# Kernel optimization log

Hardware: AMD Instinct MI355X
Metric: run time of the kernel (lower is better)

Reference implementation:

```python
import jax, jax.numpy as jnp
import numpy as np

B, N, H, D = 16, 512, 8, 128  # batch, nodes, heads, hid_dim (per-head dim == hid_dim)


def setup_inputs() -> dict:
    key = jax.random.key(0)
    ks = jax.random.split(key, 12)
    x = jax.random.normal(ks[0], (B, N, D), dtype=jnp.float32)
    dist = jax.random.normal(ks[1], (B, N, N), dtype=jnp.float32)
    mask = (jax.random.uniform(ks[2], (B, N)) < 0.9).astype(jnp.float32)
    w_std = 0.02
    Wq = jax.random.normal(ks[3], (D, H * D), dtype=jnp.float32) * w_std
    Wk = jax.random.normal(ks[4], (D, H * D), dtype=jnp.float32) * w_std
    Wv = jax.random.normal(ks[5], (D, H * D), dtype=jnp.float32) * w_std
    Wo = jax.random.normal(ks[6], (H * D, D), dtype=jnp.float32) * w_std
    bq = jax.random.normal(ks[7], (H * D,), dtype=jnp.float32) * w_std
    bk = jax.random.normal(ks[8], (H * D,), dtype=jnp.float32) * w_std
    bv = jax.random.normal(ks[9], (H * D,), dtype=jnp.float32) * w_std
    bo = jax.random.normal(ks[10], (D,), dtype=jnp.float32) * w_std
    return {"x": x, "dist": dist, "mask": mask,
            "Wq": Wq, "bq": bq, "Wk": Wk, "bk": bk,
            "Wv": Wv, "bv": bv, "Wo": Wo, "bo": bo}


def reference(x, dist, mask, Wq, bq, Wk, bk, Wv, bv, Wo, bo):
    scale = jnp.asarray(D, x.dtype) ** -0.5
    # projections: [B,N,H*D] -> [B,H,N,D]
    q = (x @ Wq + bq).reshape(B, N, H, D).transpose(0, 2, 1, 3)
    k = (x @ Wk + bk).reshape(B, N, H, D).transpose(0, 2, 1, 3)
    v = (x @ Wv + bv).reshape(B, N, H, D).transpose(0, 2, 1, 3)
    m = mask[:, None, :, None]  # [B,1,N,1]
    q = q * m * scale
    k = k * m
    v = v * m
    a = jnp.einsum('bhnd,bhmd->bhnm', q, k)  # [B,H,N,N]
    a = a + dist[:, None, :, :]  # dist bias broadcast over heads
    amask = (mask[:, :, None] * mask[:, None, :])[:, None, :, :]  # [B,1,N,N]
    a = jnp.where(amask == 0, jnp.asarray(-1e9, a.dtype), a)
    a = jax.nn.softmax(a, axis=-1)
    a = jnp.where(amask == 0, jnp.asarray(0.0, a.dtype), a)
    y = jnp.einsum('bhnm,bhmd->bhnd', a, v)
    y = y.transpose(0, 2, 1, 3).reshape(B, N, H * D)
    y = y @ Wo + bo
    return y * mask[:, :, None]
```

## Files before the change

### kernel.cpp

```cpp
#include <hip/hip_runtime.h>
#include <hip/hip_bf16.h>

#define B_ 16
#define N_ 512
#define H_ 8
#define D_ 128
#define HD_ 1024
#define SCALE_ 0.08838834764831845f

typedef __attribute__((ext_vector_type(8))) short bf16x8;
typedef __attribute__((ext_vector_type(4))) float f32x4;
typedef __attribute__((ext_vector_type(4))) _Float16 f16x4;

__device__ __forceinline__ unsigned short f2bf(float f) {
    union { __hip_bfloat16 h; unsigned short u; } cv;
    cv.h = __float2bfloat16(f);
    return cv.u;
}
__device__ __forceinline__ unsigned short f2h(float f) {
    union { _Float16 h; unsigned short u; } cv;
    cv.h = (_Float16)f;
    return cv.u;
}

#define BAR_LIGHT() do {                                     \
    asm volatile("s_waitcnt lgkmcnt(0)" ::: "memory");       \
    __builtin_amdgcn_s_barrier();                            \
    asm volatile("" ::: "memory");                           \
} while (0)

__global__ __launch_bounds__(256) void prep_kernel(
    const float* __restrict__ Wq, const float* __restrict__ Wk,
    const float* __restrict__ Wv, const float* __restrict__ Wo,
    const float* __restrict__ x,
    unsigned short* __restrict__ wTh, unsigned short* __restrict__ woT,
    unsigned short* __restrict__ xh)
{
    __shared__ float T[32][33];
    const int tile = blockIdx.x;
    const int t = threadIdx.x;
    if (tile < 384) {
        const int w = tile / 128;
        const int rem = tile % 128;
        const int kt = rem & 3;
        const int ct = rem >> 2;
        const float* W = (w == 0) ? Wq : (w == 1) ? Wk : Wv;
        const int k0 = kt * 32, c0 = ct * 32;
        #pragma unroll
        for (int u = 0; u < 4; u++) {
            int lin = t + 256 * u; int r = lin >> 5, c = lin & 31;
            T[r][c] = W[(size_t)(k0 + r) * 1024 + c0 + c];
        }
        __syncthreads();
        unsigned short* oh = wTh + (size_t)w * 131072;
        #pragma unroll
        for (int u = 0; u < 4; u++) {
            int lin = t + 256 * u; int c = lin >> 5, r = lin & 31;
            oh[(size_t)(c0 + c) * 128 + k0 + r] = f2bf(T[r][c]);
        }
    } else if (tile < 512) {
        const int rem = tile - 384;
        const int nt = rem & 3;
        const int kt = rem >> 2;
        const int k0 = kt * 32, n0 = nt * 32;
        #pragma unroll
        for (int u = 0; u < 4; u++) {
            int lin = t + 256 * u; int r = lin >> 5, c = lin & 31;
            T[r][c] = Wo[(size_t)(k0 + r) * 128 + n0 + c];
        }
        __syncthreads();
        #pragma unroll
        for (int u = 0; u < 4; u++) {
            int lin = t + 256 * u; int c = lin >> 5, r = lin & 31;
            woT[(size_t)(n0 + c) * 1024 + k0 + r] = f2bf(T[r][c]);
        }
    } else {
        const size_t base = (size_t)(tile - 512) * 2048 + (size_t)t * 8;
        float4 v0 = *(const float4*)&x[base];
        float4 v1 = *(const float4*)&x[base + 4];
        union { bf16x8 v; unsigned short s[8]; } H;
        H.s[0] = f2bf(v0.x); H.s[1] = f2bf(v0.y);
        H.s[2] = f2bf(v0.z); H.s[3] = f2bf(v0.w);
        H.s[4] = f2bf(v1.x); H.s[5] = f2bf(v1.y);
        H.s[6] = f2bf(v1.z); H.s[7] = f2bf(v1.w);
        *(bf16x8*)&xh[base] = H.v;
    }
}

__global__ __launch_bounds__(256, 3) void qkv_kernel(
    const unsigned short* __restrict__ xh, const float* __restrict__ mask,
    const unsigned short* __restrict__ wTh,
    const float* __restrict__ bq, const float* __restrict__ bk,
    const float* __restrict__ bv,
    unsigned short* __restrict__ q, unsigned short* __restrict__ k,
    unsigned short* __restrict__ vT)
{
    const int cb = blockIdx.x % 24;
    const int by = blockIdx.x / 24;
    const int row0 = by * 128, c0 = cb * 128;
    const int which = c0 >> 10, w0 = c0 & 1023;
    const float* bi = (which == 0) ? bq : (which == 1) ? bk : bv;

    __shared__ alignas(16) unsigned short Wh[128][136];
    __shared__ float biS[128];
    __shared__ float mskS[128];

    const int t = threadIdx.x;
    if (t < 128) { biS[t] = bi[w0 + t]; mskS[t] = mask[row0 + t]; }

    const unsigned short* whp = wTh + (size_t)which * 131072 + (size_t)w0 * 128;
    #pragma unroll
    for (int u = 0; u < 8; u++) {
        int lin = t + 256 * u; int c = lin >> 4, k8 = (lin & 15) * 8;
        *(bf16x8*)&Wh[c][k8] = *(const bf16x8*)&whp[(size_t)c * 128 + k8];
    }

    const int wave = t >> 6, lane = t & 63, m16 = lane & 15, g4 = lane >> 4;
    const int rw = row0 + wave * 32;

    bf16x8 ah[2][4];
    #pragma unroll
    for (int mt = 0; mt < 2; mt++)
        #pragma unroll
        for (int kc = 0; kc < 4; kc++)
            ah[mt][kc] = *(const bf16x8*)&xh[(size_t)(rw + mt * 16 + m16) * 128 + kc * 32 + g4 * 8];
    __syncthreads();

    const f32x4 zero = {0.f, 0.f, 0.f, 0.f};
    f32x4 acc[2][8];
    #pragma unroll
    for (int mt = 0; mt < 2; mt++)
        #pragma unroll
        for (int nt = 0; nt < 8; nt++) acc[mt][nt] = zero;

    #pragma unroll
    for (int nt = 0; nt < 8; nt++) {
        #pragma unroll
        for (int kc = 0; kc < 4; kc++) {
            bf16x8 bh = *(const bf16x8*)&Wh[nt * 16 + m16][kc * 32 + g4 * 8];
            #pragma unroll
            for (int mt = 0; mt < 2; mt++)
                acc[mt][nt] = __builtin_amdgcn_mfma_f32_16x16x32_bf16(ah[mt][kc], bh, acc[mt][nt], 0, 0, 0);
        }
    }
    __syncthreads();

    const int b = row0 >> 9, h = w0 >> 7;
    const int iseq0 = row0 & 511;
    unsigned short* Tr = &Wh[0][0];

    if (which == 2) {
        #pragma unroll
        for (int mt = 0; mt < 2; mt++)
            #pragma unroll
            for (int nt = 0; nt < 8; nt++)
                #pragma unroll
                for (int r = 0; r < 4; r++) {
                    int rowl = wave * 32 + mt * 16 + g4 * 4 + r;
                    int col = nt * 16 + m16;
                    Tr[col * 136 + rowl] = f2h((acc[mt][nt][r] + biS[col]) * mskS[rowl]);
                }
        __syncthreads();
        unsigned short* vbase = vT + (size_t)(b * 8 + h) * 128 * 512 + iseq0;
        #pragma unroll
        for (int u = 0; u < 8; u++) {
            int lin = t + 256 * u; int dl = lin >> 4, i8 = (lin & 15) * 8;
            *(bf16x8*)&vbase[(size_t)dl * 512 + i8] = *(const bf16x8*)&Tr[dl * 136 + i8];
        }
    } else {
        const float sc = (which == 0) ? SCALE_ : 1.0f;
        #pragma unroll
        for (int mt = 0; mt < 2; mt++)
            #pragma unroll
            for (int nt = 0; nt < 8; nt++)
                #pragma unroll
                for (int r = 0; r < 4; r++) {
                    int rowl = wave * 32 + mt * 16 + g4 * 4 + r;
                    int col = nt * 16 + m16;
                    Tr[rowl * 136 + col] = f2bf((acc[mt][nt][r] + biS[col]) * (mskS[rowl] * sc));
                }
        __syncthreads();
        unsigned short* dst = ((which == 0) ? q : k) +
                              ((size_t)(b * 8 + h) * 512 + iseq0) * 128;
        #pragma unroll
        for (int u = 0; u < 8; u++) {
            int lin = t + 256 * u; int rl = lin >> 4, c8 = (lin & 15) * 8;
            *(bf16x8*)&dst[(size_t)rl * 128 + c8] = *(const bf16x8*)&Tr[rl * 136 + c8];
        }
    }
}

__global__ __launch_bounds__(256, 2) void attn_kernel(
    const unsigned short* __restrict__ q, const unsigned short* __restrict__ k,
    const unsigned short* __restrict__ vT, const float* __restrict__ dist,
    const float* __restrict__ mask, unsigned short* __restrict__ y)
{
    const int xid = blockIdx.x;
    const int b = (xid & 7) | ((xid >> 8) << 3);
    const int itile = (xid >> 3) & 3;
    const int h = (xid >> 5) & 7;
    const int bh = b * 8 + h;
    const int i0 = itile * 128;

    const unsigned short* qb = q + (size_t)bh * 512 * 128;
    const unsigned short* kb = k + (size_t)bh * 512 * 128;
    const unsigned short* vb = vT + (size_t)bh * 128 * 512;

    __shared__ alignas(16) unsigned short Ks[2][64][136];
    __shared__ alignas(16) unsigned short Vs[2][128][76];
    __shared__ alignas(16) float cmS[512];

    const int t = threadIdx.x;
    const int wave = t >> 6, lane = t & 63;
    const int m16 = lane & 15, g4 = lane >> 4;
    const int iw = i0 + wave * 32;

    cmS[t] = (mask[b * 512 + t] == 0.0f) ? -1e9f : 0.0f;
    cmS[256 + t] = (mask[b * 512 + 256 + t] == 0.0f) ? -1e9f : 0.0f;

    bf16x8 aq0[4], aq1[4];
    #pragma unroll
    for (int c = 0; c < 4; c++) {
        aq0[c] = *(const bf16x8*)(qb + (size_t)(iw + m16) * 128 + c * 32 + g4 * 8);
        aq1[c] = *(const bf16x8*)(qb + (size_t)(iw + 16 + m16) * 128 + c * 32 + g4 * 8);
    }

    const int krow = t >> 2, kcol = (t & 3) * 32;
    const int vrow = t >> 1, vcol = (t & 1) * 32;

    const float* dbase = dist + ((size_t)b * 512 + iw) * 512;

    bf16x8 kp[4], vp[4];
    #pragma unroll
    for (int u = 0; u < 4; u++) {
        kp[u] = *(const bf16x8*)(kb + (size_t)krow * 128 + kcol + u * 8);
        vp[u] = *(const bf16x8*)(vb + (size_t)vrow * 512 + vcol + u * 8);
    }
    #pragma unroll
    for (int u = 0; u < 4; u++) {
        *(bf16x8*)&Ks[0][krow][kcol + u * 8] = kp[u];
        union { bf16x8 v8; ushort4 h4[2]; } cv; cv.v8 = vp[u];
        *(ushort4*)&Vs[0][vrow][vcol + u * 8] = cv.h4[0];
        *(ushort4*)&Vs[0][vrow][vcol + u * 8 + 4] = cv.h4[1];
    }
    BAR_LIGHT();

    const f32x4 zero = {0.f, 0.f, 0.f, 0.f};
    float rl0 = 0.f, rl1 = 0.f;
    f32x4 Ot0[8] = {zero, zero, zero, zero, zero, zero, zero, zero};
    f32x4 Ot1[8] = {zero, zero, zero, zero, zero, zero, zero, zero};

    for (int c = 0; c < 8; c++) {
        const int j0 = c * 64;
        const int bsel = c & 1;

        if (c < 7) {
            const int j0n = j0 + 64;
            #pragma unroll
            for (int u = 0; u < 4; u++) {
                kp[u] = *(const bf16x8*)(kb + (size_t)(j0n + krow) * 128 + kcol + u * 8);
                vp[u] = *(const bf16x8*)(vb + (size_t)vrow * 512 + j0n + vcol + u * 8);
            }
        }

        f32x4 dv0[4], dv1[4];
        #pragma unroll
        for (int jt = 0; jt < 4; jt++) {
            dv0[jt] = *(const f32x4*)&dbase[(size_t)m16 * 512 + j0 + jt * 16 + g4 * 4];
            dv1[jt] = *(const f32x4*)&dbase[(size_t)(16 + m16) * 512 + j0 + jt * 16 + g4 * 4];
        }

        f32x4 s0[4], s1[4];
        #pragma unroll
        for (int jt = 0; jt < 4; jt++) {
            f32x4 a0 = zero, a1 = zero;
            #pragma unroll
            for (int cc = 0; cc < 4; cc++) {
                bf16x8 kf = *(const bf16x8*)&Ks[bsel][jt * 16 + m16][cc * 32 + g4 * 8];
                a0 = __builtin_amdgcn_mfma_f32_16x16x32_bf16(kf, aq0[cc], a0, 0, 0, 0);
                a1 = __builtin_amdgcn_mfma_f32_16x16x32_bf16(kf, aq1[cc], a1, 0, 0, 0);
            }
            s0[jt] = a0; s1[jt] = a1;
        }

        f16x4 pa0[4], pa1[4];
        float ps0 = 0.f, ps1 = 0.f;
        #pragma unroll
        for (int jt = 0; jt < 4; jt++) {
            f32x4 cm4 = *(const f32x4*)&cmS[j0 + jt * 16 + g4 * 4];
            #pragma unroll
            for (int r = 0; r < 4; r++) {
                float p0 = __expf(s0[jt][r] + dv0[jt][r] + cm4[r]);
                float p1 = __expf(s1[jt][r] + dv1[jt][r] + cm4[r]);
                ps0 += p0; ps1 += p1;
                pa0[jt][r] = (_Float16)p0;
                pa1[jt][r] = (_Float16)p1;
            }
        }
        rl0 += ps0; rl1 += ps1;

        if (c < 7) {
            const int bo = bsel ^ 1;
            #pragma unroll
            for (int u = 0; u < 4; u++) {
                *(bf16x8*)&Ks[bo][krow][kcol + u * 8] = kp[u];
                union { bf16x8 v8; ushort4 h4[2]; } cv; cv.v8 = vp[u];
                *(ushort4*)&Vs[bo][vrow][vcol + u * 8] = cv.h4[0];
                *(ushort4*)&Vs[bo][vrow][vcol + u * 8 + 4] = cv.h4[1];
            }
        }

        #pragma unroll
        for (int jt = 0; jt < 4; jt++)
            #pragma unroll
            for (int dt = 0; dt < 8; dt++) {
                f16x4 vf = *(const f16x4*)&Vs[bsel][dt * 16 + m16][jt * 16 + g4 * 4];
                Ot0[dt] = __builtin_amdgcn_mfma_f32_16x16x16f16(pa0[jt], vf, Ot0[dt], 0, 0, 0);
                Ot1[dt] = __builtin_amdgcn_mfma_f32_16x16x16f16(pa1[jt], vf, Ot1[dt], 0, 0, 0);
            }

        if (c < 7) BAR_LIGHT();
    }
    BAR_LIGHT();

    rl0 += __shfl_xor(rl0, 16); rl0 += __shfl_xor(rl0, 32);
    rl1 += __shfl_xor(rl1, 16); rl1 += __shfl_xor(rl1, 32);
    float rs0 = (rl0 > 0.f) ? 1.0f / rl0 : 0.f;
    float rs1 = (rl1 > 0.f) ? 1.0f / rl1 : 0.f;
    float rs04[4], rs14[4];
    #pragma unroll
    for (int r = 0; r < 4; r++) {
        rs04[r] = __shfl(rs0, g4 * 4 + r);
        rs14[r] = __shfl(rs1, g4 * 4 + r);
    }
    unsigned short (*Sb)[136] = (wave >> 1) ? Ks[1] : Ks[0];
    const int rb = (wave & 1) * 32;
    #pragma unroll
    for (int dt = 0; dt < 8; dt++)
        #pragma unroll
        for (int r = 0; r < 4; r++) {
            Sb[rb + g4 * 4 + r][dt * 16 + m16]      = f2bf(Ot0[dt][r] * rs04[r]);
            Sb[rb + 16 + g4 * 4 + r][dt * 16 + m16] = f2bf(Ot1[dt][r] * rs14[r]);
        }
    #pragma unroll
    for (int u = 0; u < 8; u++) {
        int lin = lane + 64 * u;
        int row = lin >> 4;
        int seg = lin & 15;
        *(bf16x8*)&y[((size_t)(b * 512) + iw + row) * 1024 + h * 128 + seg * 8] =
            *(const bf16x8*)&Sb[rb + row][seg * 8];
    }
}

__global__ __launch_bounds__(256, 2) void oproj_kernel(
    const unsigned short* __restrict__ Y, const unsigned short* __restrict__ woT,
    const float* __restrict__ bo, const float* __restrict__ mask,
    float* __restrict__ out)
{
    const int row0 = blockIdx.x * 16;
    __shared__ alignas(16) unsigned short Ys[16][136];
    __shared__ alignas(16) unsigned short Ws[128][136];
    __shared__ float boS[128];
    __shared__ float mskS[16];

    const int t = threadIdx.x;
    if (t < 128) boS[t] = bo[t];
    if (t < 16) mskS[t] = mask[row0 + t];

    const int wave = t >> 6, lane = t & 63;
    const int m16 = lane & 15, g4 = lane >> 4;
    const int n0 = wave * 32;

    const int yr = t >> 4, yk = (t & 15) * 8;
    const int wn = t >> 4, wk = (t & 15) * 8;

    const f32x4 zero = {0.f, 0.f, 0.f, 0.f};
    f32x4 acc[2] = {zero, zero};

    bf16x8 yp, wp[8];
    yp = *(const bf16x8*)&Y[(size_t)(row0 + yr) * 1024 + yk];
    #pragma unroll
    for (int u = 0; u < 8; u++)
        wp[u] = *(const bf16x8*)&woT[(size_t)(wn + u * 16) * 1024 + wk];

    for (int c = 0; c < 8; c++) {
        __syncthreads();
        *(bf16x8*)&Ys[yr][yk] = yp;
        #pragma unroll
        for (int u = 0; u < 8; u++) *(bf16x8*)&Ws[wn + u * 16][wk] = wp[u];
        __syncthreads();
        if (c < 7) {
            const int kc0 = (c + 1) * 128;
            yp = *(const bf16x8*)&Y[(size_t)(row0 + yr) * 1024 + kc0 + yk];
            #pragma unroll
            for (int u = 0; u < 8; u++)
                wp[u] = *(const bf16x8*)&woT[(size_t)(wn + u * 16) * 1024 + kc0 + wk];
        }
        #pragma unroll
        for (int kc = 0; kc < 4; kc++) {
            bf16x8 a = *(const bf16x8*)&Ys[m16][kc * 32 + g4 * 8];
            #pragma unroll
            for (int nt = 0; nt < 2; nt++) {
                bf16x8 bb = *(const bf16x8*)&Ws[n0 + nt * 16 + m16][kc * 32 + g4 * 8];
                acc[nt] = __builtin_amdgcn_mfma_f32_16x16x32_bf16(a, bb, acc[nt], 0, 0, 0);
            }
        }
    }
    __syncthreads();

    float* Ot = (float*)&Ws[0][0];
    #pragma unroll
    for (int nt = 0; nt < 2; nt++)
        #pragma unroll
        for (int r = 0; r < 4; r++) {
            int rowl = g4 * 4 + r;
            int col = n0 + nt * 16 + m16;
            Ot[rowl * 132 + col] = (acc[nt][r] + boS[col]) * mskS[rowl];
        }
    __syncthreads();
    #pragma unroll
    for (int u = 0; u < 2; u++) {
        int lin = t + 256 * u; int r = lin >> 5, c4 = lin & 31;
        *(float4*)&out[(size_t)(row0 + r) * 128 + c4 * 4] =
            *(const float4*)&Ot[r * 132 + c4 * 4];
    }
}

extern "C" void kernel_launch(void* const* d_in, const int* in_sizes, int n_in,
                              void* d_out, int out_size, void* d_ws, size_t ws_size,
                              hipStream_t stream) {
    const float* x    = (const float*)d_in[0];
    const float* dist = (const float*)d_in[1];
    const float* mask = (const float*)d_in[2];
    const float* Wq   = (const float*)d_in[3];
    const float* bq   = (const float*)d_in[4];
    const float* Wk   = (const float*)d_in[5];
    const float* bk   = (const float*)d_in[6];
    const float* Wv   = (const float*)d_in[7];
    const float* bv   = (const float*)d_in[8];
    const float* Wo   = (const float*)d_in[9];
    const float* bo   = (const float*)d_in[10];
    float* out = (float*)d_out;

    const size_t perE = (size_t)B_ * H_ * N_ * D_;
    unsigned short* qb  = (unsigned short*)d_ws;
    unsigned short* kb  = qb + perE;
    unsigned short* vb  = kb + perE;
    unsigned short* yb  = vb + perE;
    unsigned short* wTh = yb + perE;
    unsigned short* woT = wTh + 3 * 131072;
    unsigned short* xh  = yb;

    prep_kernel<<<1024, 256, 0, stream>>>(Wq, Wk, Wv, Wo, x, wTh, woT, xh);
    qkv_kernel<<<1536, 256, 0, stream>>>(xh, mask, wTh, bq, bk, bv, qb, kb, vb);
    attn_kernel<<<512, 256, 0, stream>>>(qb, kb, vb, dist, mask, yb);
    oproj_kernel<<<512, 256, 0, stream>>>(yb, woT, bo, mask, out);
}
```

Baseline: 145.1 us.

## Double oproj row tile and load Y fragments directly from global

The output-projection kernel now handles 32 rows per block instead of 16, so each staged Wo tile in shared memory feeds twice as many MFMAs and only half as many blocks are launched. The Y tile is no longer staged through shared memory: each wave loads its A fragments straight from global memory into registers. Barriers switch to a BAR_LIGHT macro and launch bounds are raised to 3 blocks per CU. The trade-offs are duplicated global reads of Y across the four waves, more registers per thread, and only 256 blocks to spread across the GPU.

Measured after the change: 150.0 us. 3.3% more time.

```diff
diff --git a/kernel.cpp b/kernel.cpp
--- a/kernel.cpp
+++ b/kernel.cpp
@@ -352,74 +352,81 @@
     }
 }
 
-__global__ __launch_bounds__(256, 2) void oproj_kernel(
+__global__ __launch_bounds__(256, 3) void oproj_kernel(
     const unsigned short* __restrict__ Y, const unsigned short* __restrict__ woT,
     const float* __restrict__ bo, const float* __restrict__ mask,
     float* __restrict__ out)
 {
-    const int row0 = blockIdx.x * 16;
-    __shared__ alignas(16) unsigned short Ys[16][136];
+    const int row0 = blockIdx.x * 32;
     __shared__ alignas(16) unsigned short Ws[128][136];
     __shared__ float boS[128];
-    __shared__ float mskS[16];
+    __shared__ float mskS[32];
 
     const int t = threadIdx.x;
     if (t < 128) boS[t] = bo[t];
-    if (t < 16) mskS[t] = mask[row0 + t];
+    if (t < 32) mskS[t] = mask[row0 + t];
 
     const int wave = t >> 6, lane = t & 63;
     const int m16 = lane & 15, g4 = lane >> 4;
     const int n0 = wave * 32;
 
-    const int yr = t >> 4, yk = (t & 15) * 8;
     const int wn = t >> 4, wk = (t & 15) * 8;
 
     const f32x4 zero = {0.f, 0.f, 0.f, 0.f};
-    f32x4 acc[2] = {zero, zero};
-
-    bf16x8 yp, wp[8];
-    yp = *(const bf16x8*)&Y[(size_t)(row0 + yr) * 1024 + yk];
+    f32x4 acc[2][2] = {{zero, zero}, {zero, zero}};
+
+    bf16x8 wp[8];
     #pragma unroll
     for (int u = 0; u < 8; u++)
         wp[u] = *(const bf16x8*)&woT[(size_t)(wn + u * 16) * 1024 + wk];
 
     for (int c = 0; c < 8; c++) {
-        __syncthreads();
-        *(bf16x8*)&Ys[yr][yk] = yp;
+        const int kc0 = c * 128;
+        BAR_LIGHT();
         #pragma unroll
         for (int u = 0; u < 8; u++) *(bf16x8*)&Ws[wn + u * 16][wk] = wp[u];
-        __syncthreads();
+
+        bf16x8 ah[2][4];
+        #pragma unroll
+        for (int mt = 0; mt < 2; mt++)
+            #pragma unroll
+            for (int kc = 0; kc < 4; kc++)
+                ah[mt][kc] = *(const bf16x8*)&Y[(size_t)(row0 + mt * 16 + m16) * 1024 + kc0 + kc * 32 + g4 * 8];
+
         if (c < 7) {
-            const int kc0 = (c + 1) * 128;
-            yp = *(const bf16x8*)&Y[(size_t)(row0 + yr) * 1024 + kc0 + yk];
+            const int kn = kc0 + 128;
             #pragma unroll
             for (int u = 0; u < 8; u++)
-                wp[u] = *(const bf16x8*)&woT[(size_t)(wn + u * 16) * 1024 + kc0 + wk];
-        }
-        #pragma unroll
-        for (int kc = 0; kc < 4; kc++) {
-            bf16x8 a = *(const bf16x8*)&Ys[m16][kc * 32 + g4 * 8];
+                wp[u] = *(const bf16x8*)&woT[(size_t)(wn + u * 16) * 1024 + kn + wk];
+        }
+        BAR_LIGHT();
+
+        #pragma unroll
+        for (int kc = 0; kc < 4; kc++)
             #pragma unroll
             for (int nt = 0; nt < 2; nt++) {
                 bf16x8 bb = *(const bf16x8*)&Ws[n0 + nt * 16 + m16][kc * 32 + g4 * 8];
-                acc[nt] = __builtin_amdgcn_mfma_f32_16x16x32_bf16(a, bb, acc[nt], 0, 0, 0);
-            }
-        }
-    }
-    __syncthreads();
+                #pragma unroll
+                for (int mt = 0; mt < 2; mt++)
+                    acc[mt][nt] = __builtin_amdgcn_mfma_f32_16x16x32_bf16(ah[mt][kc], bb, acc[mt][nt], 0, 0, 0);
+            }
+    }
+    BAR_LIGHT();
 
     float* Ot = (float*)&Ws[0][0];
     #pragma unroll
-    for (int nt = 0; nt < 2; nt++)
-        #pragma unroll
-        for (int r = 0; r < 4; r++) {
-            int rowl = g4 * 4 + r;
-            int col = n0 + nt * 16 + m16;
-            Ot[rowl * 132 + col] = (acc[nt][r] + boS[col]) * mskS[rowl];
-        }
-    __syncthreads();
-    #pragma unroll
-    for (int u = 0; u < 2; u++) {
+    for (int mt = 0; mt < 2; mt++)
+        #pragma unroll
+        for (int nt = 0; nt < 2; nt++)
+            #pragma unroll
+            for (int r = 0; r < 4; r++) {
+                int rowl = mt * 16 + g4 * 4 + r;
+                int col = n0 + nt * 16 + m16;
+                Ot[rowl * 132 + col] = (acc[mt][nt][r] + boS[col]) * mskS[rowl];
+            }
+    BAR_LIGHT();
+    #pragma unroll
+    for (int u = 0; u < 4; u++) {
         int lin = t + 256 * u; int r = lin >> 5, c4 = lin & 31;
         *(float4*)&out[(size_t)(row0 + r) * 128 + c4 * 4] =
             *(const float4*)&Ot[r * 132 + c4 * 4];
@@ -454,5 +461,5 @@
     prep_kernel<<<1024, 256, 0, stream>>>(Wq, Wk, Wv, Wo, x, wTh, woT, xh);
     qkv_kernel<<<1536, 256, 0, stream>>>(xh, mask, wTh, bq, bk, bv, qb, kb, vb);
     attn_kernel<<<512, 256, 0, stream>>>(qb, kb, vb, dist, mask, yb);
-    oproj_kernel<<<512, 256, 0, stream>>>(yb, woT, bo, mask, out);
-}
+    oproj_kernel<<<256, 256, 0, stream>>>(yb, woT, bo, mask, out);
+}
```
